# Optimization experiments

Measured on AMD Instinct MI355X. Metric: run time of the kernel, lower is better.

Reference implementation:

```python
import jax, jax.numpy as jnp
import numpy as np

N_WRD = 2000
WCODE = 3
EMB = 32
VSIZE = 7
VIEW = (16, 16)
B = 64
CSIZE = 128


def _vcode():
    # torch.meshgrid with default 'ij' indexing, cat -> (2, H*W) -> (H*W, 2)
    x = jnp.linspace(-1.0, 1.0, VIEW[0])
    y = jnp.linspace(-1.0, 1.0, VIEW[1])
    xg, yg = jnp.meshgrid(x, y, indexing='ij')
    return jnp.stack([xg.reshape(-1), yg.reshape(-1)], axis=-1)  # (V, 2)


def setup_inputs() -> dict:
    key = jax.random.key(0)
    ks = jax.random.split(key, 20)
    s = 0.02
    d = {
        'view_cell': jax.random.normal(ks[0], (B, CSIZE, VIEW[0] * VIEW[1]), jnp.float32),
        'v': jax.random.normal(ks[1], (B, VSIZE), jnp.float32),
        'w2c_w1': jax.random.normal(ks[2], (VSIZE, 512), jnp.float32) * s,
        'w2c_b1': jnp.zeros((512,), jnp.float32),
        'w2c_w2': jax.random.normal(ks[3], (512, WCODE * N_WRD), jnp.float32) * s,
        'w2c_b2': jnp.zeros((WCODE * N_WRD,), jnp.float32),
        'fc1_w': jax.random.normal(ks[4], (WCODE, 256), jnp.float32) * s,
        'fc1_b': jnp.zeros((256,), jnp.float32),
        'fc2_w': jax.random.normal(ks[5], (256, 256), jnp.float32) * s,
        'fc2_b': jnp.zeros((256,), jnp.float32),
        'fca_w': jax.random.normal(ks[6], (256, 1), jnp.float32) * s,
        'fca_b': jnp.zeros((1,), jnp.float32),
        'fce_w': jax.random.normal(ks[7], (256, EMB), jnp.float32) * s,
        'fce_b': jnp.zeros((EMB,), jnp.float32),
        'vse_w1': jax.random.normal(ks[8], (2, 128), jnp.float32) * s,
        'vse_b1': jnp.zeros((128,), jnp.float32),
        'vse_w2': jax.random.normal(ks[9], (128, EMB), jnp.float32) * s,
        'vse_b2': jnp.zeros((EMB,), jnp.float32),
    }
    return d


def reference(view_cell, v, w2c_w1, w2c_b1, w2c_w2, w2c_b2,
              fc1_w, fc1_b, fc2_w, fc2_b, fca_w, fca_b, fce_w, fce_b,
              vse_w1, vse_b1, vse_w2, vse_b2):
    b = v.shape[0]
    # w2c: v -> per-cell world codes
    h0 = jax.nn.relu(v @ w2c_w1 + w2c_b1)                     # (B, 512)
    wcode = (h0 @ w2c_w2 + w2c_b2).reshape(-1, WCODE)          # (B*N, 3)
    h = jax.nn.relu(wcode @ fc1_w + fc1_b)                     # (B*N, 256)
    h = jax.nn.relu(h @ fc2_w + fc2_b)
    activation = jax.nn.sigmoid(h @ fca_w + fca_b).reshape(b, N_WRD, 1)
    cs_emb = (h @ fce_w + fce_b).reshape(b, N_WRD, EMB)        # (B, N, E)
    # view-space embedding of the pixel grid
    vcode = _vcode()                                           # (V, 2)
    vs = jax.nn.relu(vcode @ vse_w1 + vse_b1) @ vse_w2 + vse_b2  # (V, E)
    # relation / gated softmax routing
    relation = jnp.einsum('bne,ve->bnv', cs_emb, vs)           # (B, N, V)
    route = jax.nn.softmax(relation, axis=2) * activation      # (B, N, V)
    # write: view_cell (B, C, V) @ route^T (B, V, N) -> (B, C, N)
    wrd_cell = jnp.einsum('bcv,bnv->bcn', view_cell, route)
    return wrd_cell
```

## Files before the change

kernel.cpp:

```cpp
#include <hip/hip_runtime.h>
#include <hip/hip_bf16.h>
#include <math.h>

#define NWRD 2000

typedef __attribute__((ext_vector_type(8)))  short short8;
typedef __attribute__((ext_vector_type(16))) float f32x16;

#define WS_FC2WT 0
#define WS_WCODE (WS_FC2WT + 32768)
#define WS_VSB   (WS_WCODE + 384000)
#define WS_W2T   (WS_VSB + 4096)
#define WS_VCB   (WS_W2T + 1536000)
#define WS_FCEWT (WS_VCB + 1048576)
#define WS_H0B   (WS_FCEWT + 4096)
#define WS_FCAWB (WS_H0B + 16384)

__device__ __forceinline__ unsigned short f2bf(float x) {
    unsigned int u = __float_as_uint(x);
    u += 0x7fffu + ((u >> 16) & 1u);
    return (unsigned short)(u >> 16);
}
__device__ __forceinline__ unsigned int pkbf(float lo, float hi) {
    unsigned int r;
    asm("v_cvt_pk_bf16_f32 %0, %1, %2" : "=v"(r) : "v"(lo), "v"(hi));
    return r;
}

#define PR_K2  94
#define PR_VCB (PR_K2 + 1024)
#define PR_VSB (PR_VCB + 32)
#define PR_FC2 (PR_VSB + 16)
#define PREP_N (PR_FC2 + 1)
__global__ __launch_bounds__(256) void kprep(
        const float* __restrict__ vc, unsigned short* __restrict__ vcb,
        const float* __restrict__ w2,
        const float* __restrict__ v, const float* __restrict__ w1,
        const float* __restrict__ b1, const float* __restrict__ b2,
        float* __restrict__ wcode,
        const float* __restrict__ vse_w1, const float* __restrict__ vse_b1,
        const float* __restrict__ vse_w2, const float* __restrict__ vse_b2,
        unsigned short* __restrict__ vsb,
        const float* __restrict__ fc2_w, unsigned short* __restrict__ fc2wT,
        const float* __restrict__ fce_w, unsigned short* __restrict__ fcewT,
        const float* __restrict__ fca_w, unsigned short* __restrict__ fcawB) {
    __shared__ __align__(16) unsigned short smem[10240];
    int bid = blockIdx.x, t = threadIdx.x;
    if (bid < PR_K2) {
        unsigned short* ha = smem;
        unsigned short* wb = smem + 4608;
        int n0 = bid * 64;
        int w = t >> 6, lane = t & 63, l31 = lane & 31, h = lane >> 5;
        int mt = w & 1, nt = w >> 1;
        int kk = t & 63, mg = t >> 6;
        int colc = n0 + kk; if (colc > 5999) colc = 5999;
        f32x16 acc;
#pragma unroll
        for (int i = 0; i < 16; i++) acc[i] = 0.f;
        for (int p = 0; p < 8; p++) {
            int k0 = p * 64;
            float w1c[7];
#pragma unroll
            for (int q = 0; q < 7; q++) w1c[q] = w1[q*512 + k0 + kk];
            float bbv = b1[k0 + kk];
#pragma unroll
            for (int mm = 0; mm < 16; mm++) {
                int m = mg*16 + mm;
                float s = bbv;
#pragma unroll
                for (int q = 0; q < 7; q++) s = fmaf(v[m*7 + q], w1c[q], s);
                ha[m*72 + kk] = f2bf(fmaxf(s, 0.f));
            }
#pragma unroll
            for (int i = 0; i < 16; i++)
                wb[kk*72 + mg*16 + i] = f2bf(w2[(size_t)(k0 + mg*16 + i)*6000 + colc]);
            __syncthreads();
#pragma unroll
            for (int ks = 0; ks < 4; ks++) {
                short8 af = *(const short8*)(ha + (mt*32 + l31)*72 + ks*16 + h*8);
                short8 bf = *(const short8*)(wb + (nt*32 + l31)*72 + ks*16 + h*8);
                acc = __builtin_amdgcn_mfma_f32_32x32x16_bf16(af, bf, acc, 0, 0, 0);
            }
            __syncthreads();
        }
        int n = n0 + nt*32 + l31;
        if (n < 6000) {
            float bias = b2[n];
#pragma unroll
            for (int i = 0; i < 16; i++) {
                int row = (i & 3) + 8*(i >> 2) + 4*h;
                wcode[(size_t)(mt*32 + row)*6000 + n] = acc[i] + bias;
            }
        }
    } else if (bid < PR_VCB) {
        int i = ((bid - PR_K2) * 256 + t) * 8;
        float4 f0 = *(const float4*)(vc + i);
        float4 f1 = *(const float4*)(vc + i + 4);
        union { short8 v8; unsigned int u[4]; } o;
        o.u[0] = pkbf(f0.x, f0.y); o.u[1] = pkbf(f0.z, f0.w);
        o.u[2] = pkbf(f1.x, f1.y); o.u[3] = pkbf(f1.z, f1.w);
        *(short8*)(vcb + i) = o.v8;
    } else if (bid < PR_VSB) {
        float* hs = (float*)smem;
        int blk = bid - PR_VCB;
        int m = t & 127, half = t >> 7;
#pragma unroll
        for (int q = 0; q < 4; q++) {
            int vloc = half*4 + q;
            int vv = blk*8 + vloc;
            float x = (2.f/15.f)*(float)(vv >> 4) - 1.f;
            float y = (2.f/15.f)*(float)(vv & 15) - 1.f;
            float hh = vse_b1[m] + x*vse_w1[m] + y*vse_w1[128 + m];
            hs[vloc*128 + m] = fmaxf(hh, 0.f);
        }
        __syncthreads();
        int vloc = t >> 5, e = t & 31;
        float s = vse_b2[e];
        for (int mm = 0; mm < 128; mm++) s = fmaf(hs[vloc*128 + mm], vse_w2[mm*32 + e], s);
        vsb[(blk*8 + vloc)*32 + e] = f2bf(s);
    } else if (bid < PR_FC2) {
        unsigned short (*tile)[72] = (unsigned short(*)[72])smem;
        int b2t = bid - PR_VSB;
        int k0t = (b2t >> 2) * 64, n0t = (b2t & 3) * 64;
        int nl = t & 63, kb = (t >> 6) * 16;
#pragma unroll
        for (int i = 0; i < 16; i++)
            tile[kb + i][nl] = f2bf(fc2_w[(size_t)(k0t + kb + i)*256 + n0t + nl]);
        __syncthreads();
        int kl = t & 63, nb = (t >> 6) * 16;
#pragma unroll
        for (int i = 0; i < 16; i++)
            fc2wT[(size_t)(n0t + nb + i)*256 + k0t + kl] = tile[kl][nb + i];
    } else {
        int e = t & 31, kb = (t >> 5) * 32;
        unsigned short tmp[32];
#pragma unroll
        for (int i = 0; i < 32; i++) tmp[i] = f2bf(fce_w[(size_t)(kb + i)*32 + e]);
#pragma unroll
        for (int i = 0; i < 4; i++)
            *(short8*)(fcewT + (size_t)e*256 + kb + i*8) = *(short8*)(tmp + i*8);
#pragma unroll
        for (int i = 0; i < 32; i++)
            fcawB[(size_t)e*256 + kb + i] = (e == 0) ? f2bf(fca_w[kb + i]) : (unsigned short)0;
    }
}

#define K45_LDS 43264
__device__ __forceinline__ void fc1_row(const float* __restrict__ wr,
        const float4& wa, const float4& wb4, const float4& wc, const float4& bb4,
        unsigned short* dst) {
    float c0 = wr[0], c1 = wr[1], c2 = wr[2];
    float v0 = fmaxf(fmaf(c2, wc.x, fmaf(c1, wb4.x, fmaf(c0, wa.x, bb4.x))), 0.f);
    float v1 = fmaxf(fmaf(c2, wc.y, fmaf(c1, wb4.y, fmaf(c0, wa.y, bb4.y))), 0.f);
    float v2 = fmaxf(fmaf(c2, wc.z, fmaf(c1, wb4.z, fmaf(c0, wa.z, bb4.z))), 0.f);
    float v3 = fmaxf(fmaf(c2, wc.w, fmaf(c1, wb4.w, fmaf(c0, wa.w, bb4.w))), 0.f);
    uint2 p;
    p.x = pkbf(v0, v1);
    p.y = pkbf(v2, v3);
    *(uint2*)dst = p;
}
__global__ __launch_bounds__(512, 4) void k45(
        const unsigned short* __restrict__ vcb,
        const float* __restrict__ wcode,
        const float* __restrict__ fc1_w, const float* __restrict__ fc1_b,
        const unsigned short* __restrict__ fc2wT, const float* __restrict__ fc2_b,
        const float* __restrict__ fca_b_p,
        const unsigned short* __restrict__ fcawB,
        const unsigned short* __restrict__ fcewT, const float* __restrict__ fce_b,
        const unsigned short* __restrict__ vsb,
        float* __restrict__ out) {
    extern __shared__ char lds[];
    unsigned short* buf   = (unsigned short*)lds;
    unsigned short* embL  = (unsigned short*)(lds + 33792);
    float* wcsAll = (float*)(lds + 38912);
    float* redS   = (float*)(lds + 41984);
    float* actL   = (float*)(lds + 43008);
    int t = threadIdx.x;
    int w = t >> 6, lane = t & 63, l31 = lane & 31, h = lane >> 5;
    int b = blockIdx.y;
    int n0 = blockIdx.x * 256;

    {
        const float* wsrc = wcode + (size_t)b*6000;
        int i0 = n0*3 + t;
        wcsAll[t] = wsrc[i0 < 6000 ? i0 : 5999];
        if (t < 256) {
            int i1 = n0*3 + 512 + t;
            wcsAll[512 + t] = wsrc[i1 < 6000 ? i1 : 5999];
        }
    }
    int jq = (t & 63) * 4;
    int mtF = w & 1, nqF = w >> 1;
    int colA = nqF*64 + l31, colB = colA + 32;
    float baA = fc2_b[colA], baB = fc2_b[colB];
    float be = fce_b[l31];
    float fcab = fca_b_p[0];
    int ntR = w & 1, vq = w >> 1;
    int cq = w >> 1, ntE = w & 1;
    size_t arowE = ((size_t)(b*128 + cq*32 + l31))*256;
    __syncthreads();

    for (int c = 0; c < 4; c++) {
        {
            float4 wa  = *(const float4*)(fc1_w + jq);
            float4 wb4 = *(const float4*)(fc1_w + 256 + jq);
            float4 wc  = *(const float4*)(fc1_w + 512 + jq);
            float4 bb4 = *(const float4*)(fc1_b + jq);
#pragma unroll
            for (int rr = 0; rr < 8; rr++) {
                int r = w*8 + rr;
                fc1_row(wcsAll + (c*64 + r)*3, wa, wb4, wc, bb4, buf + r*264 + jq);
            }
        }
        __syncthreads();
        f32x16 c0, c1;
#pragma unroll
        for (int i = 0; i < 16; i++) { c0[i] = 0.f; c1[i] = 0.f; }
#pragma unroll 4
        for (int ks = 0; ks < 16; ks++) {
            int k0 = ks*16 + h*8;
            short8 af  = *(const short8*)(buf + (mtF*32 + l31)*264 + k0);
            short8 bf0 = *(const short8*)(fc2wT + (size_t)colA*256 + k0);
            short8 bf1 = *(const short8*)(fc2wT + (size_t)colB*256 + k0);
            c0 = __builtin_amdgcn_mfma_f32_32x32x16_bf16(af, bf0, c0, 0, 0, 0);
            c1 = __builtin_amdgcn_mfma_f32_32x32x16_bf16(af, bf1, c1, 0, 0, 0);
        }
        __syncthreads();
#pragma unroll
        for (int i = 0; i < 16; i++) {
            int row = (i & 3) + 8*(i >> 2) + 4*h;
            unsigned int pk = pkbf(fmaxf(c0[i] + baA, 0.f), fmaxf(c1[i] + baB, 0.f));
            buf[(mtF*32 + row)*264 + colA] = (unsigned short)pk;
            buf[(mtF*32 + row)*264 + colB] = (unsigned short)(pk >> 16);
        }
        __syncthreads();
        if (w < 2) {
            f32x16 ce;
#pragma unroll
            for (int i = 0; i < 16; i++) ce[i] = 0.f;
#pragma unroll 4
            for (int ks = 0; ks < 16; ks++) {
                int k0 = ks*16 + h*8;
                short8 af = *(const short8*)(buf + (w*32 + l31)*264 + k0);
                short8 bf = *(const short8*)(fcewT + (size_t)l31*256 + k0);
                ce = __builtin_amdgcn_mfma_f32_32x32x16_bf16(af, bf, ce, 0, 0, 0);
            }
#pragma unroll
            for (int i = 0; i < 16; i += 2) {
                int row = (i & 3) + 8*(i >> 2) + 4*h;
                unsigned int pk = pkbf(ce[i] + be, ce[i+1] + be);
                embL[(w*32 + row)*40 + l31]     = (unsigned short)pk;
                embL[(w*32 + row + 1)*40 + l31] = (unsigned short)(pk >> 16);
            }
        } else if (w < 4) {
            int m = w - 2;
            f32x16 ca;
#pragma unroll
            for (int i = 0; i < 16; i++) ca[i] = 0.f;
#pragma unroll 4
            for (int ks = 0; ks < 16; ks++) {
                int k0 = ks*16 + h*8;
                short8 af = *(const short8*)(buf + (m*32 + l31)*264 + k0);
                short8 bf = *(const short8*)(fcawB + (size_t)l31*256 + k0);
                ca = __builtin_amdgcn_mfma_f32_32x32x16_bf16(af, bf, ca, 0, 0, 0);
            }
            if (l31 == 0) {
#pragma unroll
                for (int i = 0; i < 16; i++) {
                    int row = (i & 3) + 8*(i >> 2) + 4*h;
                    actL[m*32 + row] = ca[i];
                }
            }
        }
        __syncthreads();
        {
            int nloc = ntR*32 + l31;
            f32x16 ra[2];
#pragma unroll
            for (int mt = 0; mt < 2; mt++)
#pragma unroll
                for (int i = 0; i < 16; i++) ra[mt][i] = 0.f;
#pragma unroll
            for (int s = 0; s < 2; s++) {
                short8 bfrag = *(const short8*)(embL + nloc*40 + s*16 + h*8);
#pragma unroll
                for (int mt = 0; mt < 2; mt++) {
                    int vrow = (vq*2 + mt)*32 + l31;
                    short8 afrag = *(const short8*)(vsb + vrow*32 + s*16 + h*8);
                    ra[mt] = __builtin_amdgcn_mfma_f32_32x32x16_bf16(afrag, bfrag, ra[mt], 0, 0, 0);
                }
            }
            float sm = 0.f;
#pragma unroll
            for (int mt = 0; mt < 2; mt++)
#pragma unroll
                for (int i = 0; i < 16; i++) {
                    float e = __expf(ra[mt][i]);
                    ra[mt][i] = e;
                    sm += e;
                }
            sm += __shfl_xor(sm, 32);
            if (lane < 32) redS[w*32 + l31] = sm;
#pragma unroll
            for (int mt = 0; mt < 2; mt++) {
#pragma unroll
                for (int g = 0; g < 4; g++) {
                    int vb = (vq*2 + mt)*32 + 8*g + 4*h;
                    unsigned int p0 = pkbf(ra[mt][g*4+0], ra[mt][g*4+1]);
                    unsigned int p1 = pkbf(ra[mt][g*4+2], ra[mt][g*4+3]);
                    *(uint2*)(buf + nloc*264 + vb) = make_uint2(p0, p1);
                }
            }
        }
        __syncthreads();
        {
            f32x16 cc;
#pragma unroll
            for (int i = 0; i < 16; i++) cc[i] = 0.f;
            const unsigned short* rrow = buf + (ntE*32 + l31)*264;
#pragma unroll 4
            for (int ks = 0; ks < 16; ks++) {
                int k0 = ks*16 + h*8;
                short8 bf = *(const short8*)(rrow + k0);
                short8 a0 = *(const short8*)(vcb + arowE + k0);
                cc = __builtin_amdgcn_mfma_f32_32x32x16_bf16(a0, bf, cc, 0, 0, 0);
            }
            int wloc = ntE*32 + l31;
            float smt = 0.f;
#pragma unroll
            for (int q = 0; q < 4; q++) smt += redS[(q*2 + ntE)*32 + l31];
            float al = actL[wloc] + fcab;
            float scale = (1.f / (1.f + __expf(-al))) / smt;
            int ng = n0 + c*64 + wloc;
            if (ng < NWRD) {
                float* ob = out + (size_t)b*128*NWRD + ng;
#pragma unroll
                for (int i = 0; i < 16; i++) {
                    int crow = (i & 3) + 8*(i >> 2) + 4*h;
                    __builtin_nontemporal_store(cc[i]*scale,
                                                ob + (size_t)(cq*32 + crow)*NWRD);
                }
            }
        }
        if (c < 3) __syncthreads();
    }
}

extern "C" void kernel_launch(void* const* d_in, const int* in_sizes, int n_in,
                              void* d_out, int out_size, void* d_ws, size_t ws_size,
                              hipStream_t stream) {
    const float* view_cell = (const float*)d_in[0];
    const float* v       = (const float*)d_in[1];
    const float* w2c_w1  = (const float*)d_in[2];
    const float* w2c_b1  = (const float*)d_in[3];
    const float* w2c_w2  = (const float*)d_in[4];
    const float* w2c_b2  = (const float*)d_in[5];
    const float* fc1_w   = (const float*)d_in[6];
    const float* fc1_b   = (const float*)d_in[7];
    const float* fc2_w   = (const float*)d_in[8];
    const float* fc2_b   = (const float*)d_in[9];
    const float* fca_w   = (const float*)d_in[10];
    const float* fca_b   = (const float*)d_in[11];
    const float* fce_w   = (const float*)d_in[12];
    const float* fce_b   = (const float*)d_in[13];
    const float* vse_w1  = (const float*)d_in[14];
    const float* vse_b1  = (const float*)d_in[15];
    const float* vse_w2  = (const float*)d_in[16];
    const float* vse_b2  = (const float*)d_in[17];
    float* ws    = (float*)d_ws;
    unsigned short* fc2wT = (unsigned short*)(ws + WS_FC2WT);
    float* wcode = ws + WS_WCODE;
    unsigned short* vsb   = (unsigned short*)(ws + WS_VSB);
    unsigned short* vcb   = (unsigned short*)(ws + WS_VCB);
    unsigned short* fcewT = (unsigned short*)(ws + WS_FCEWT);
    unsigned short* fcawB = (unsigned short*)(ws + WS_FCAWB);
    float* out   = (float*)d_out;

    kprep<<<PREP_N, 256, 0, stream>>>(view_cell, vcb,
                                      w2c_w2, v, w2c_w1, w2c_b1, w2c_b2, wcode,
                                      vse_w1, vse_b1, vse_w2, vse_b2, vsb,
                                      fc2_w, fc2wT, fce_w, fcewT, fca_w, fcawB);
    (void)hipFuncSetAttribute((const void*)k45,
                              hipFuncAttributeMaxDynamicSharedMemorySize, K45_LDS);
    dim3 g45(8, 64);
    k45<<<g45, 512, K45_LDS, stream>>>(vcb, wcode, fc1_w, fc1_b, fc2wT, fc2_b,
                                       fca_b, fcawB, fcewT, fce_b, vsb, out);
}
```

Baseline: 233.4 us.

## Split k45 into one 64-word chunk per block, quadrupling grid size

The fused k45 kernel no longer loops over four 64-word chunks per block. Each block now handles a single chunk, so the grid grows from 8x64 to 32x64. The wcode staging in LDS is dropped and fc1 reads wcode directly from global memory, which shrinks LDS use. This trades more blocks, which should fill the CUs better, for redundant per-block setup: the vcb A-tile rows, fc2wT and the bias loads are re-read once per chunk instead of once per four chunks.

```diff
diff --git a/kernel.cpp b/kernel.cpp
--- a/kernel.cpp
+++ b/kernel.cpp
@@ -145,20 +145,7 @@
     }
 }
 
-#define K45_LDS 43264
-__device__ __forceinline__ void fc1_row(const float* __restrict__ wr,
-        const float4& wa, const float4& wb4, const float4& wc, const float4& bb4,
-        unsigned short* dst) {
-    float c0 = wr[0], c1 = wr[1], c2 = wr[2];
-    float v0 = fmaxf(fmaf(c2, wc.x, fmaf(c1, wb4.x, fmaf(c0, wa.x, bb4.x))), 0.f);
-    float v1 = fmaxf(fmaf(c2, wc.y, fmaf(c1, wb4.y, fmaf(c0, wa.y, bb4.y))), 0.f);
-    float v2 = fmaxf(fmaf(c2, wc.z, fmaf(c1, wb4.z, fmaf(c0, wa.z, bb4.z))), 0.f);
-    float v3 = fmaxf(fmaf(c2, wc.w, fmaf(c1, wb4.w, fmaf(c0, wa.w, bb4.w))), 0.f);
-    uint2 p;
-    p.x = pkbf(v0, v1);
-    p.y = pkbf(v2, v3);
-    *(uint2*)dst = p;
-}
+#define K45_LDS 40192
 __global__ __launch_bounds__(512, 4) void k45(
         const unsigned short* __restrict__ vcb,
         const float* __restrict__ wcode,
@@ -172,23 +159,13 @@
     extern __shared__ char lds[];
     unsigned short* buf   = (unsigned short*)lds;
     unsigned short* embL  = (unsigned short*)(lds + 33792);
-    float* wcsAll = (float*)(lds + 38912);
-    float* redS   = (float*)(lds + 41984);
-    float* actL   = (float*)(lds + 43008);
+    float* redS   = (float*)(lds + 38912);
+    float* actL   = (float*)(lds + 39936);
     int t = threadIdx.x;
     int w = t >> 6, lane = t & 63, l31 = lane & 31, h = lane >> 5;
     int b = blockIdx.y;
-    int n0 = blockIdx.x * 256;
-
-    {
-        const float* wsrc = wcode + (size_t)b*6000;
-        int i0 = n0*3 + t;
-        wcsAll[t] = wsrc[i0 < 6000 ? i0 : 5999];
-        if (t < 256) {
-            int i1 = n0*3 + 512 + t;
-            wcsAll[512 + t] = wsrc[i1 < 6000 ? i1 : 5999];
-        }
-    }
+    int n0 = blockIdx.x * 64;
+
     int jq = (t & 63) * 4;
     int mtF = w & 1, nqF = w >> 1;
     int colA = nqF*64 + l31, colB = colA + 32;
@@ -198,151 +175,157 @@
     int ntR = w & 1, vq = w >> 1;
     int cq = w >> 1, ntE = w & 1;
     size_t arowE = ((size_t)(b*128 + cq*32 + l31))*256;
-    __syncthreads();
-
-    for (int c = 0; c < 4; c++) {
-        {
-            float4 wa  = *(const float4*)(fc1_w + jq);
-            float4 wb4 = *(const float4*)(fc1_w + 256 + jq);
-            float4 wc  = *(const float4*)(fc1_w + 512 + jq);
-            float4 bb4 = *(const float4*)(fc1_b + jq);
-#pragma unroll
-            for (int rr = 0; rr < 8; rr++) {
-                int r = w*8 + rr;
-                fc1_row(wcsAll + (c*64 + r)*3, wa, wb4, wc, bb4, buf + r*264 + jq);
-            }
-        }
-        __syncthreads();
-        f32x16 c0, c1;
-#pragma unroll
-        for (int i = 0; i < 16; i++) { c0[i] = 0.f; c1[i] = 0.f; }
+
+    {
+        float4 wa  = *(const float4*)(fc1_w + jq);
+        float4 wb4 = *(const float4*)(fc1_w + 256 + jq);
+        float4 wc  = *(const float4*)(fc1_w + 512 + jq);
+        float4 bb4 = *(const float4*)(fc1_b + jq);
+        const float* wrow = wcode + (size_t)b*6000;
+#pragma unroll
+        for (int rr = 0; rr < 8; rr++) {
+            int r = w*8 + rr;
+            int i = (n0 + r)*3; if (i > 5997) i = 5997;
+            float c0 = wrow[i], c1 = wrow[i+1], c2 = wrow[i+2];
+            float v0 = fmaxf(fmaf(c2, wc.x, fmaf(c1, wb4.x, fmaf(c0, wa.x, bb4.x))), 0.f);
+            float v1 = fmaxf(fmaf(c2, wc.y, fmaf(c1, wb4.y, fmaf(c0, wa.y, bb4.y))), 0.f);
+            float v2 = fmaxf(fmaf(c2, wc.z, fmaf(c1, wb4.z, fmaf(c0, wa.z, bb4.z))), 0.f);
+            float v3 = fmaxf(fmaf(c2, wc.w, fmaf(c1, wb4.w, fmaf(c0, wa.w, bb4.w))), 0.f);
+            uint2 p;
+            p.x = pkbf(v0, v1);
+            p.y = pkbf(v2, v3);
+            *(uint2*)(buf + r*264 + jq) = p;
+        }
+    }
+    __syncthreads();
+    f32x16 c0a, c1a;
+#pragma unroll
+    for (int i = 0; i < 16; i++) { c0a[i] = 0.f; c1a[i] = 0.f; }
+#pragma unroll 4
+    for (int ks = 0; ks < 16; ks++) {
+        int k0 = ks*16 + h*8;
+        short8 af  = *(const short8*)(buf + (mtF*32 + l31)*264 + k0);
+        short8 bf0 = *(const short8*)(fc2wT + (size_t)colA*256 + k0);
+        short8 bf1 = *(const short8*)(fc2wT + (size_t)colB*256 + k0);
+        c0a = __builtin_amdgcn_mfma_f32_32x32x16_bf16(af, bf0, c0a, 0, 0, 0);
+        c1a = __builtin_amdgcn_mfma_f32_32x32x16_bf16(af, bf1, c1a, 0, 0, 0);
+    }
+    __syncthreads();
+#pragma unroll
+    for (int i = 0; i < 16; i++) {
+        int row = (i & 3) + 8*(i >> 2) + 4*h;
+        unsigned int pk = pkbf(fmaxf(c0a[i] + baA, 0.f), fmaxf(c1a[i] + baB, 0.f));
+        buf[(mtF*32 + row)*264 + colA] = (unsigned short)pk;
+        buf[(mtF*32 + row)*264 + colB] = (unsigned short)(pk >> 16);
+    }
+    __syncthreads();
+    if (w < 2) {
+        f32x16 ce;
+#pragma unroll
+        for (int i = 0; i < 16; i++) ce[i] = 0.f;
 #pragma unroll 4
         for (int ks = 0; ks < 16; ks++) {
             int k0 = ks*16 + h*8;
-            short8 af  = *(const short8*)(buf + (mtF*32 + l31)*264 + k0);
-            short8 bf0 = *(const short8*)(fc2wT + (size_t)colA*256 + k0);
-            short8 bf1 = *(const short8*)(fc2wT + (size_t)colB*256 + k0);
-            c0 = __builtin_amdgcn_mfma_f32_32x32x16_bf16(af, bf0, c0, 0, 0, 0);
-            c1 = __builtin_amdgcn_mfma_f32_32x32x16_bf16(af, bf1, c1, 0, 0, 0);
-        }
-        __syncthreads();
-#pragma unroll
-        for (int i = 0; i < 16; i++) {
+            short8 af = *(const short8*)(buf + (w*32 + l31)*264 + k0);
+            short8 bf = *(const short8*)(fcewT + (size_t)l31*256 + k0);
+            ce = __builtin_amdgcn_mfma_f32_32x32x16_bf16(af, bf, ce, 0, 0, 0);
+        }
+#pragma unroll
+        for (int i = 0; i < 16; i += 2) {
             int row = (i & 3) + 8*(i >> 2) + 4*h;
-            unsigned int pk = pkbf(fmaxf(c0[i] + baA, 0.f), fmaxf(c1[i] + baB, 0.f));
-            buf[(mtF*32 + row)*264 + colA] = (unsigned short)pk;
-            buf[(mtF*32 + row)*264 + colB] = (unsigned short)(pk >> 16);
-        }
-        __syncthreads();
-        if (w < 2) {
-            f32x16 ce;
-#pragma unroll
-            for (int i = 0; i < 16; i++) ce[i] = 0.f;
+            unsigned int pk = pkbf(ce[i] + be, ce[i+1] + be);
+            embL[(w*32 + row)*40 + l31]     = (unsigned short)pk;
+            embL[(w*32 + row + 1)*40 + l31] = (unsigned short)(pk >> 16);
+        }
+    } else if (w < 4) {
+        int m = w - 2;
+        f32x16 ca;
+#pragma unroll
+        for (int i = 0; i < 16; i++) ca[i] = 0.f;
 #pragma unroll 4
-            for (int ks = 0; ks < 16; ks++) {
-                int k0 = ks*16 + h*8;
-                short8 af = *(const short8*)(buf + (w*32 + l31)*264 + k0);
-                short8 bf = *(const short8*)(fcewT + (size_t)l31*256 + k0);
-                ce = __builtin_amdgcn_mfma_f32_32x32x16_bf16(af, bf, ce, 0, 0, 0);
-            }
-#pragma unroll
-            for (int i = 0; i < 16; i += 2) {
+        for (int ks = 0; ks < 16; ks++) {
+            int k0 = ks*16 + h*8;
+            short8 af = *(const short8*)(buf + (m*32 + l31)*264 + k0);
+            short8 bf = *(const short8*)(fcawB + (size_t)l31*256 + k0);
+            ca = __builtin_amdgcn_mfma_f32_32x32x16_bf16(af, bf, ca, 0, 0, 0);
+        }
+        if (l31 == 0) {
+#pragma unroll
+            for (int i = 0; i < 16; i++) {
                 int row = (i & 3) + 8*(i >> 2) + 4*h;
-                unsigned int pk = pkbf(ce[i] + be, ce[i+1] + be);
-                embL[(w*32 + row)*40 + l31]     = (unsigned short)pk;
-                embL[(w*32 + row + 1)*40 + l31] = (unsigned short)(pk >> 16);
-            }
-        } else if (w < 4) {
-            int m = w - 2;
-            f32x16 ca;
-#pragma unroll
-            for (int i = 0; i < 16; i++) ca[i] = 0.f;
+                actL[m*32 + row] = ca[i];
+            }
+        }
+    }
+    __syncthreads();
+    {
+        int nloc = ntR*32 + l31;
+        f32x16 ra[2];
+#pragma unroll
+        for (int mt = 0; mt < 2; mt++)
+#pragma unroll
+            for (int i = 0; i < 16; i++) ra[mt][i] = 0.f;
+#pragma unroll
+        for (int s = 0; s < 2; s++) {
+            short8 bfrag = *(const short8*)(embL + nloc*40 + s*16 + h*8);
+#pragma unroll
+            for (int mt = 0; mt < 2; mt++) {
+                int vrow = (vq*2 + mt)*32 + l31;
+                short8 afrag = *(const short8*)(vsb + vrow*32 + s*16 + h*8);
+                ra[mt] = __builtin_amdgcn_mfma_f32_32x32x16_bf16(afrag, bfrag, ra[mt], 0, 0, 0);
+            }
+        }
+        float sm = 0.f;
+#pragma unroll
+        for (int mt = 0; mt < 2; mt++)
+#pragma unroll
+            for (int i = 0; i < 16; i++) {
+                float e = __expf(ra[mt][i]);
+                ra[mt][i] = e;
+                sm += e;
+            }
+        sm += __shfl_xor(sm, 32);
+        if (lane < 32) redS[w*32 + l31] = sm;
+#pragma unroll
+        for (int mt = 0; mt < 2; mt++) {
+#pragma unroll
+            for (int g = 0; g < 4; g++) {
+                int vb = (vq*2 + mt)*32 + 8*g + 4*h;
+                unsigned int p0 = pkbf(ra[mt][g*4+0], ra[mt][g*4+1]);
+                unsigned int p1 = pkbf(ra[mt][g*4+2], ra[mt][g*4+3]);
+                *(uint2*)(buf + nloc*264 + vb) = make_uint2(p0, p1);
+            }
+        }
+    }
+    __syncthreads();
+    {
+        f32x16 cc;
+#pragma unroll
+        for (int i = 0; i < 16; i++) cc[i] = 0.f;
+        const unsigned short* rrow = buf + (ntE*32 + l31)*264;
 #pragma unroll 4
-            for (int ks = 0; ks < 16; ks++) {
-                int k0 = ks*16 + h*8;
-                short8 af = *(const short8*)(buf + (m*32 + l31)*264 + k0);
-                short8 bf = *(const short8*)(fcawB + (size_t)l31*256 + k0);
-                ca = __builtin_amdgcn_mfma_f32_32x32x16_bf16(af, bf, ca, 0, 0, 0);
-            }
-            if (l31 == 0) {
-#pragma unroll
-                for (int i = 0; i < 16; i++) {
-                    int row = (i & 3) + 8*(i >> 2) + 4*h;
-                    actL[m*32 + row] = ca[i];
-                }
-            }
-        }
-        __syncthreads();
-        {
-            int nloc = ntR*32 + l31;
-            f32x16 ra[2];
-#pragma unroll
-            for (int mt = 0; mt < 2; mt++)
-#pragma unroll
-                for (int i = 0; i < 16; i++) ra[mt][i] = 0.f;
-#pragma unroll
-            for (int s = 0; s < 2; s++) {
-                short8 bfrag = *(const short8*)(embL + nloc*40 + s*16 + h*8);
-#pragma unroll
-                for (int mt = 0; mt < 2; mt++) {
-                    int vrow = (vq*2 + mt)*32 + l31;
-                    short8 afrag = *(const short8*)(vsb + vrow*32 + s*16 + h*8);
-                    ra[mt] = __builtin_amdgcn_mfma_f32_32x32x16_bf16(afrag, bfrag, ra[mt], 0, 0, 0);
-                }
-            }
-            float sm = 0.f;
-#pragma unroll
-            for (int mt = 0; mt < 2; mt++)
-#pragma unroll
-                for (int i = 0; i < 16; i++) {
-                    float e = __expf(ra[mt][i]);
-                    ra[mt][i] = e;
-                    sm += e;
-                }
-            sm += __shfl_xor(sm, 32);
-            if (lane < 32) redS[w*32 + l31] = sm;
-#pragma unroll
-            for (int mt = 0; mt < 2; mt++) {
-#pragma unroll
-                for (int g = 0; g < 4; g++) {
-                    int vb = (vq*2 + mt)*32 + 8*g + 4*h;
-                    unsigned int p0 = pkbf(ra[mt][g*4+0], ra[mt][g*4+1]);
-                    unsigned int p1 = pkbf(ra[mt][g*4+2], ra[mt][g*4+3]);
-                    *(uint2*)(buf + nloc*264 + vb) = make_uint2(p0, p1);
-                }
-            }
-        }
-        __syncthreads();
-        {
-            f32x16 cc;
-#pragma unroll
-            for (int i = 0; i < 16; i++) cc[i] = 0.f;
-            const unsigned short* rrow = buf + (ntE*32 + l31)*264;
-#pragma unroll 4
-            for (int ks = 0; ks < 16; ks++) {
-                int k0 = ks*16 + h*8;
-                short8 bf = *(const short8*)(rrow + k0);
-                short8 a0 = *(const short8*)(vcb + arowE + k0);
-                cc = __builtin_amdgcn_mfma_f32_32x32x16_bf16(a0, bf, cc, 0, 0, 0);
-            }
-            int wloc = ntE*32 + l31;
-            float smt = 0.f;
-#pragma unroll
-            for (int q = 0; q < 4; q++) smt += redS[(q*2 + ntE)*32 + l31];
-            float al = actL[wloc] + fcab;
-            float scale = (1.f / (1.f + __expf(-al))) / smt;
-            int ng = n0 + c*64 + wloc;
-            if (ng < NWRD) {
-                float* ob = out + (size_t)b*128*NWRD + ng;
-#pragma unroll
-                for (int i = 0; i < 16; i++) {
-                    int crow = (i & 3) + 8*(i >> 2) + 4*h;
-                    __builtin_nontemporal_store(cc[i]*scale,
-                                                ob + (size_t)(cq*32 + crow)*NWRD);
-                }
-            }
-        }
-        if (c < 3) __syncthreads();
+        for (int ks = 0; ks < 16; ks++) {
+            int k0 = ks*16 + h*8;
+            short8 bf = *(const short8*)(rrow + k0);
+            short8 a0 = *(const short8*)(vcb + arowE + k0);
+            cc = __builtin_amdgcn_mfma_f32_32x32x16_bf16(a0, bf, cc, 0, 0, 0);
+        }
+        int wloc = ntE*32 + l31;
+        float smt = 0.f;
+#pragma unroll
+        for (int q = 0; q < 4; q++) smt += redS[(q*2 + ntE)*32 + l31];
+        float al = actL[wloc] + fcab;
+        float scale = (1.f / (1.f + __expf(-al))) / smt;
+        int ng = n0 + wloc;
+        if (ng < NWRD) {
+            float* ob = out + (size_t)b*128*NWRD + ng;
+#pragma unroll
+            for (int i = 0; i < 16; i++) {
+                int crow = (i & 3) + 8*(i >> 2) + 4*h;
+                __builtin_nontemporal_store(cc[i]*scale,
+                                            ob + (size_t)(cq*32 + crow)*NWRD);
+            }
+        }
     }
 }
 
@@ -382,7 +365,7 @@
                                       fc2_w, fc2wT, fce_w, fcewT, fca_w, fcawB);
     (void)hipFuncSetAttribute((const void*)k45,
                               hipFuncAttributeMaxDynamicSharedMemorySize, K45_LDS);
-    dim3 g45(8, 64);
+    dim3 g45(32, 64);
     k45<<<g45, 512, K45_LDS, stream>>>(vcb, wcode, fc1_w, fc1_b, fc2wT, fc2_b,
                                        fca_b, fcawB, fcewT, fce_b, vsb, out);
 }
```

After: 235.1 us. No clear change (+0.7%).
